# Kernel tuning notes

Measured on AMD Instinct MI355X. Metric: run time of the kernel, lower is better.

## Reference

```python
import jax, jax.numpy as jnp
import numpy as np
import math

N_PATHS = 2048
N_STEPS = 512
N_FWD = 40
N_FACTORS = 3
H = 0.1
ALPHA = H - 0.5            # fBM kernel exponent
BETA_SABR = 0.5
SHIFT = 0.02
DT = 1.0 / N_STEPS
GAMMA_CONST = math.gamma(H + 0.5)
BETA_DECAY = 0.05


def setup_inputs() -> dict:
    key = jax.random.key(0)
    tenors = np.linspace(0.0, 10.0, N_FWD + 1)
    T = tenors[:-1]
    tau = np.diff(tenors).astype(np.float32)
    F0 = np.full(N_FWD, 0.02, dtype=np.float32)
    # alphas = base normal vols / |F0+shift|^beta  (as in __init__)
    base_vols = np.full(N_FWD, 0.006)
    eta_F0 = np.abs(F0 + SHIFT) ** BETA_SABR
    alphas = (base_vols / eta_F0).astype(np.float32)
    rhos = np.full(N_FWD, -0.3, dtype=np.float32)
    nus = np.full(N_FWD, 0.5, dtype=np.float32)
    # PCA loadings from exponential spatial correlation (as in __init__)
    corr = np.exp(-BETA_DECAY * np.abs(T[:, None] - T[None, :]))
    evals, evecs = np.linalg.eigh(corr)
    idx = np.argsort(evals)[::-1][:N_FACTORS]
    L = evecs[:, idx] * np.sqrt(np.clip(evals[idx], 0.0, None))[None, :]
    L = L / np.sqrt((L ** 2).sum(axis=1, keepdims=True))
    Lam = np.triu(L @ L.T, 1).astype(np.float32)
    # Brownian increments, pre-scaled by sqrt(dt) (replaces Sobol+icdf draw)
    dz = jax.random.normal(key, (N_PATHS, N_STEPS, N_FACTORS + 1), dtype=jnp.float32) * float(np.sqrt(DT))
    return {
        "dz_all": dz,
        "F0": jnp.asarray(F0),
        "alphas": jnp.asarray(alphas),
        "rhos": jnp.asarray(rhos),
        "nus": jnp.asarray(nus),
        "tau": jnp.asarray(tau),
        "loadings": jnp.asarray(L.astype(np.float32)),
        "Lambda_upper": jnp.asarray(Lam),
    }


def reference(dz_all, F0, alphas, rhos, nus, tau, loadings, Lambda_upper):
    n_paths, n_steps, _ = dz_all.shape
    dtype = dz_all.dtype
    # --- hybrid-scheme Volterra / fBM kernel [n_steps, n_steps] ---
    idx = jnp.arange(n_steps)
    k = jnp.maximum(idx[:, None] - idx[None, :] + 1, 0).astype(dtype)
    # with b_eval='optimal', riemann == exact weights, so the where(k<=kappa) is identity
    exact_w = (k ** (ALPHA + 1.0) - jnp.maximum(k - 1.0, 0.0) ** (ALPHA + 1.0)) / (ALPHA + 1.0)
    kernel = jnp.where(idx[:, None] >= idx[None, :], exact_w * (DT ** ALPHA) / GAMMA_CONST, 0.0)
    # variance compensator [N, n_steps]
    var_comp = 0.5 * (nus ** 2)[:, None] * jnp.sum(kernel ** 2, axis=1)[None, :] * DT
    # --- correlated Brownian drivers and fBM via kernel convolution ---
    wr = jnp.einsum('psf,nf->psn', dz_all[..., :N_FACTORS], loadings)          # [P,S,N]
    fbm4 = jnp.einsum('ts,psd->ptd', kernel, dz_all)                            # [P,S,4]
    fbm_curve = jnp.einsum('ptf,nf->ptn', fbm4[..., :N_FACTORS], loadings)      # [P,S,N]
    fbm = rhos * fbm_curve + jnp.sqrt(1.0 - rhos ** 2) * fbm4[..., -1:]
    unit_vols = jnp.exp(nus * fbm - var_comp.T[None])                            # [P,S,N]
    v2_dt = unit_vols ** 2 * DT
    # --- frozen-drift forward dynamics ---
    eta_f0 = jnp.abs(F0 + SHIFT) ** BETA_SABR
    vol_scale = alphas * eta_f0
    omega_0 = tau * vol_scale / (1.0 + tau * F0)
    mu_0 = -vol_scale * (Lambda_upper @ omega_0)
    dF = mu_0 * v2_dt + wr * (unit_vols * vol_scale)
    F_path = F0 + jnp.cumsum(dF, axis=1)                                         # [P,S,N]
    return jnp.concatenate([jnp.broadcast_to(F0, (n_paths, 1, F0.shape[0])), F_path], axis=1)
```

## Files before the change

kernel.cpp:

```cpp
#include <hip/hip_runtime.h>
#include <math.h>

#define NS 512
#define NF 40
#define ROWS_OUT 513
#define DTC (1.0f / 512.0f)
#define PLANE 512


__global__ __launch_bounds__(64) void const_kernel(
    const float* __restrict__ F0, const float* __restrict__ alphas,
    const float* __restrict__ rhos, const float* __restrict__ nus,
    const float* __restrict__ tau, const float* __restrict__ L,
    const float* __restrict__ Lam, float* __restrict__ ws)
{
    __shared__ double wd[NS];
    __shared__ float omega0[NF];
    __shared__ float vs_s[NF];
    int n = threadIdx.x;

    {
        const double g06 = 1.4891922488128171;
        const double dta = pow(512.0, 0.4);
        #pragma unroll
        for (int k = 0; k < 8; ++k) {
            int m = n * 8 + k;
            double wv = (pow((double)m + 1.0, 0.6) - pow((double)m, 0.6)) * (1.0 / 0.6) * dta / g06;
            wd[m] = wv;
            ws[m] = (float)wv;
        }
    }
    if (n < NF) {
        float f0 = F0[n];
        float vs = alphas[n] * sqrtf(fabsf(f0 + 0.02f));
        vs_s[n] = vs;
        omega0[n] = tau[n] * vs / (1.0f + tau[n] * f0);
    }
    __syncthreads();
    if (n == 0) {
        double acc = 0.0;
        for (int m = 0; m < NS; ++m) { acc += wd[m] * wd[m]; ws[NS + m] = (float)acc; }
    }
    if (n < NF) {
        float s = 0.0f;
        for (int j = 0; j < NF; ++j) s += Lam[n * NF + j] * omega0[j];
        float vs = vs_s[n];
        float mu0 = -vs * s;
        float rho = rhos[n], nu = nus[n];
        float* c = ws + 1024 + n * 8;
        c[0] = vs * L[n * 3 + 0];
        c[1] = vs * L[n * 3 + 1];
        c[2] = vs * L[n * 3 + 2];
        c[3] = nu * rho / fmaxf(vs, 1e-30f);
        c[4] = nu * sqrtf(fmaxf(1.0f - rho * rho, 0.0f));
        c[5] = 0.5f * nu * nu * DTC;
        c[6] = mu0 * DTC;
        c[7] = F0[n];
    }
}

template<int CTRL, int RM>
__device__ __forceinline__ float dpp_add(float v) {
    int t = __builtin_amdgcn_update_dpp(0, __float_as_int(v), CTRL, RM, 0xf, true);
    return v + __int_as_float(t);
}
__device__ __forceinline__ float wave_iscan(float v) {
    v = dpp_add<0x111, 0xf>(v);
    v = dpp_add<0x112, 0xf>(v);
    v = dpp_add<0x114, 0xf>(v);
    v = dpp_add<0x118, 0xf>(v);
    v = dpp_add<0x142, 0xa>(v);
    v = dpp_add<0x143, 0xc>(v);
    return v;
}

__device__ __forceinline__ void fma4(float4& acc, float c, const float4& v) {
    acc.x = fmaf(c, v.x, acc.x);
    acc.y = fmaf(c, v.y, acc.y);
    acc.z = fmaf(c, v.z, acc.z);
    acc.w = fmaf(c, v.w, acc.w);
}

__global__ __launch_bounds__(256, 8) void path_kernel(
    const float* __restrict__ dz, const float* __restrict__ ws,
    float* __restrict__ out)
{
    __shared__ float planes[4 * PLANE];
    __shared__ float ustage[64 * 41];

    int tid = threadIdx.x;
    int lane = tid & 63;
    int wv = __builtin_amdgcn_readfirstlane(tid >> 6);
    int p = blockIdx.x;
    const float4* dzg = (const float4*)dz + (size_t)p * NS;

    float* wp = ustage;
    for (int i = tid; i < 768; i += 256) wp[i] = (i < 256) ? 0.0f : ws[i - 256];
    __syncthreads();

    {
        int role = (wv + p) & 3;
        int half = role >> 1;
        int seg  = role & 1;
        int i = half * 64 + lane;
        int span = half ? 64 : 32;
        int g0 = seg * span, g1 = g0 + span;
        const float4* wp4 = (const float4*)wp;
        float4 a0 = make_float4(0.f, 0.f, 0.f, 0.f);
        float4 a1 = a0, a2 = a0, a3 = a0;
        #pragma unroll 2
        for (int g = g0; g < g1; ++g) {
            float4 d0 = dzg[4 * g + 0];
            float4 d1 = dzg[4 * g + 1];
            float4 d2 = dzg[4 * g + 2];
            float4 d3 = dzg[4 * g + 3];
            float4 lo = wp4[63 + i - g];
            float4 hi = wp4[64 + i - g];
            fma4(a0, hi.x, d0); fma4(a1, hi.y, d0); fma4(a2, hi.z, d0); fma4(a3, hi.w, d0);
            fma4(a0, lo.w, d1); fma4(a1, hi.x, d1); fma4(a2, hi.y, d1); fma4(a3, hi.z, d1);
            fma4(a0, lo.z, d2); fma4(a1, lo.w, d2); fma4(a2, hi.x, d2); fma4(a3, hi.y, d2);
            fma4(a0, lo.y, d3); fma4(a1, lo.z, d3); fma4(a2, lo.w, d3); fma4(a3, hi.x, d3);
        }
        if (seg == 1) {
            ((float4*)(planes + 0 * PLANE))[i] = make_float4(a0.x, a1.x, a2.x, a3.x);
            ((float4*)(planes + 1 * PLANE))[i] = make_float4(a0.y, a1.y, a2.y, a3.y);
            ((float4*)(planes + 2 * PLANE))[i] = make_float4(a0.z, a1.z, a2.z, a3.z);
            ((float4*)(planes + 3 * PLANE))[i] = make_float4(a0.w, a1.w, a2.w, a3.w);
        }
        __syncthreads();
        if (seg == 0) {
            float4* q0 = &((float4*)(planes + 0 * PLANE))[i];
            float4* q1 = &((float4*)(planes + 1 * PLANE))[i];
            float4* q2 = &((float4*)(planes + 2 * PLANE))[i];
            float4* q3 = &((float4*)(planes + 3 * PLANE))[i];
            float4 c0 = *q0, c1 = *q1, c2 = *q2, c3 = *q3;
            c0.x += a0.x; c0.y += a1.x; c0.z += a2.x; c0.w += a3.x;
            c1.x += a0.y; c1.y += a1.y; c1.z += a2.y; c1.w += a3.y;
            c2.x += a0.z; c2.y += a1.z; c2.z += a2.z; c2.w += a3.z;
            c3.x += a0.w; c3.y += a1.w; c3.z += a2.w; c3.w += a3.w;
            *q0 = c0; *q1 = c1; *q2 = c2; *q3 = c3;
        }
        __syncthreads();
    }

    float carry[10];
    #pragma unroll
    for (int j = 0; j < 10; ++j) carry[j] = 0.0f;

    float* outP = out + (size_t)p * (ROWS_OUT * NF);
    if (tid < NF) outP[tid] = ws[1024 + tid * 8 + 7];

    float* chunk = ustage;
    const float* cwg = ws + NS;
    for (int cix = 0; cix < 8; ++cix) {
        int t = cix * 64 + lane;
        float cw = cwg[t];
        float fx = planes[t], fy = planes[PLANE + t];
        float fz = planes[2 * PLANE + t], fw = planes[3 * PLANE + t];
        float4 d = dzg[t];
        #pragma unroll
        for (int j = 0; j < 10; ++j) {
            int n = wv * 10 + j;
            const float* c = ws + 1024 + n * 8;
            float cC0 = c[0], cC1 = c[1], cC2 = c[2], q = c[3];
            float cA3 = c[4], ca = c[5], cm0 = c[6], f0 = c[7];
            float dotf = fx * cC0 + fy * cC1 + fz * cC2;
            float arg = fmaf(q, dotf, fmaf(cA3, fw, -ca * cw));
            float uv = __expf(arg);
            float dotc = d.x * cC0 + d.y * cC1 + d.z * cC2;
            float dF = uv * fmaf(cm0, uv, dotc);
            float v = wave_iscan(dF) + carry[j];
            carry[j] = __int_as_float(__builtin_amdgcn_readlane(__float_as_int(v), 63));
            chunk[lane * 41 + n] = v + f0;
        }
        __syncthreads();
        float* o = outP + NF + cix * (64 * NF);
        #pragma unroll
        for (int k = 0; k < 10; ++k) {
            int f = tid + k * 256;
            __builtin_nontemporal_store(chunk[f + f / 40], o + f);
        }
        __syncthreads();
    }
}

extern "C" void kernel_launch(void* const* d_in, const int* in_sizes, int n_in,
                              void* d_out, int out_size, void* d_ws, size_t ws_size,
                              hipStream_t stream) {
    const float* dz   = (const float*)d_in[0];
    const float* F0   = (const float*)d_in[1];
    const float* alph = (const float*)d_in[2];
    const float* rhos = (const float*)d_in[3];
    const float* nus  = (const float*)d_in[4];
    const float* tau  = (const float*)d_in[5];
    const float* L    = (const float*)d_in[6];
    const float* Lam  = (const float*)d_in[7];
    float* ws = (float*)d_ws;
    float* out = (float*)d_out;

    int n_paths = in_sizes[0] / (NS * 4);

    const_kernel<<<1, 64, 0, stream>>>(F0, alph, rhos, nus, tau, L, Lam, ws);
    path_kernel<<<n_paths, 256, 0, stream>>>(dz, ws, out);
}
```

Measured before the change: 256.2 us.

## Compute fBM kernel convolution with bf16 MFMA over a materialized Toeplitz matrix

```diff
diff --git a/kernel.cpp b/kernel.cpp
--- a/kernel.cpp
+++ b/kernel.cpp
@@ -7,6 +7,15 @@
 #define DTC (1.0f / 512.0f)
 #define PLANE 512
 
+typedef short bf16x8 __attribute__((ext_vector_type(8)));
+typedef float f32x4 __attribute__((ext_vector_type(4)));
+
+#define W_BYTES_NEEDED (1344u * 4u + 512u * 512u * 2u)
+
+__device__ __forceinline__ unsigned short f2bf(float x) {
+    unsigned int u = __float_as_uint(x);
+    return (unsigned short)((u + 0x7FFFu + ((u >> 16) & 1u)) >> 16);
+}
 
 __global__ __launch_bounds__(64) void const_kernel(
     const float* __restrict__ F0, const float* __restrict__ alphas,
@@ -18,7 +27,6 @@
     __shared__ float omega0[NF];
     __shared__ float vs_s[NF];
     int n = threadIdx.x;
-
     {
         const double g06 = 1.4891922488128171;
         const double dta = pow(512.0, 0.4);
@@ -59,6 +67,19 @@
     }
 }
 
+__global__ __launch_bounds__(128) void toeplitz_kernel(float* __restrict__ ws)
+{
+    int t = blockIdx.x;
+    int s0 = threadIdx.x * 4;
+    ushort4 v;
+    v.x = (s0 + 0 <= t) ? f2bf(ws[t - s0 - 0]) : (unsigned short)0;
+    v.y = (s0 + 1 <= t) ? f2bf(ws[t - s0 - 1]) : (unsigned short)0;
+    v.z = (s0 + 2 <= t) ? f2bf(ws[t - s0 - 2]) : (unsigned short)0;
+    v.w = (s0 + 3 <= t) ? f2bf(ws[t - s0 - 3]) : (unsigned short)0;
+    ushort4* W = (ushort4*)((unsigned short*)(ws + 1344) + (size_t)t * 512);
+    W[threadIdx.x] = v;
+}
+
 template<int CTRL, int RM>
 __device__ __forceinline__ float dpp_add(float v) {
     int t = __builtin_amdgcn_update_dpp(0, __float_as_int(v), CTRL, RM, 0xf, true);
@@ -79,6 +100,105 @@
     acc.y = fmaf(c, v.y, acc.y);
     acc.z = fmaf(c, v.z, acc.z);
     acc.w = fmaf(c, v.w, acc.w);
+}
+
+__global__ __launch_bounds__(256, 8) void path_kernel_mfma(
+    const float* __restrict__ dz, const float* __restrict__ ws,
+    float* __restrict__ out)
+{
+    __shared__ float planes[NS * 4];
+    __shared__ float ustage[64 * 41];
+
+    int tid = threadIdx.x;
+    int lane = tid & 63;
+    int wv = __builtin_amdgcn_readfirstlane(tid >> 6);
+    int p = blockIdx.x;
+    const float4* dzg = (const float4*)dz + (size_t)p * NS;
+
+    unsigned short* dzb = (unsigned short*)ustage;
+    {
+        int k2 = tid * 2;
+        float4 da = dzg[k2], db = dzg[k2 + 1];
+        unsigned int* d32 = (unsigned int*)dzb;
+        d32[0 * 256 + tid] = (unsigned int)f2bf(da.x) | ((unsigned int)f2bf(db.x) << 16);
+        d32[1 * 256 + tid] = (unsigned int)f2bf(da.y) | ((unsigned int)f2bf(db.y) << 16);
+        d32[2 * 256 + tid] = (unsigned int)f2bf(da.z) | ((unsigned int)f2bf(db.z) << 16);
+        d32[3 * 256 + tid] = (unsigned int)f2bf(da.w) | ((unsigned int)f2bf(db.w) << 16);
+    }
+    __syncthreads();
+
+    {
+        const unsigned short* W = (const unsigned short*)(ws + 1344);
+        int arow = lane & 15, ksub = lane >> 4;
+        f32x4 acc[8];
+        #pragma unroll
+        for (int j = 0; j < 8; ++j) acc[j] = (f32x4){0.f, 0.f, 0.f, 0.f};
+        const unsigned short* bbase = dzb + (lane & 3) * 512 + ksub * 8;
+        #pragma unroll 1
+        for (int k = 0; k < 16; ++k) {
+            bf16x8 bf = *(const bf16x8*)(bbase + k * 32);
+            #pragma unroll
+            for (int j = 0; j < 8; ++j) {
+                int m = wv + 4 * j;
+                if (k <= ((16 * m + 15) >> 5)) {
+                    bf16x8 af = *(const bf16x8*)(W + (size_t)(16 * m + arow) * NS + k * 32 + ksub * 8);
+                    acc[j] = __builtin_amdgcn_mfma_f32_16x16x32_bf16(af, bf, acc[j], 0, 0, 0);
+                }
+            }
+        }
+        if (arow < 4) {
+            #pragma unroll
+            for (int j = 0; j < 8; ++j) {
+                int m = wv + 4 * j;
+                #pragma unroll
+                for (int r = 0; r < 4; ++r)
+                    planes[(16 * m + ksub * 4 + r) * 4 + arow] = acc[j][r];
+            }
+        }
+    }
+
+    float carry[10];
+    #pragma unroll
+    for (int j = 0; j < 10; ++j) carry[j] = 0.0f;
+
+    float* outP = out + (size_t)p * (ROWS_OUT * NF);
+    if (tid < NF) outP[tid] = ws[1024 + tid * 8 + 7];
+
+    __syncthreads();
+
+    float* chunk = ustage;
+    const float* cwg = ws + NS;
+    const float4* planes4 = (const float4*)planes;
+    for (int cix = 0; cix < 8; ++cix) {
+        int t = cix * 64 + lane;
+        float cw = cwg[t];
+        float4 f4 = planes4[t];
+        float fx = f4.x, fy = f4.y, fz = f4.z, fw = f4.w;
+        float4 d = dzg[t];
+        #pragma unroll
+        for (int j = 0; j < 10; ++j) {
+            int n = wv * 10 + j;
+            const float* c = ws + 1024 + n * 8;
+            float cC0 = c[0], cC1 = c[1], cC2 = c[2], q = c[3];
+            float cA3 = c[4], ca = c[5], cm0 = c[6], f0 = c[7];
+            float dotf = fx * cC0 + fy * cC1 + fz * cC2;
+            float arg = fmaf(q, dotf, fmaf(cA3, fw, -ca * cw));
+            float uv = __expf(arg);
+            float dotc = d.x * cC0 + d.y * cC1 + d.z * cC2;
+            float dF = uv * fmaf(cm0, uv, dotc);
+            float v = wave_iscan(dF) + carry[j];
+            carry[j] = __int_as_float(__builtin_amdgcn_readlane(__float_as_int(v), 63));
+            chunk[lane * 41 + n] = v + f0;
+        }
+        __syncthreads();
+        float* o = outP + NF + cix * (64 * NF);
+        #pragma unroll
+        for (int k = 0; k < 10; ++k) {
+            int f = tid + k * 256;
+            __builtin_nontemporal_store(chunk[f + f / 40], o + f);
+        }
+        __syncthreads();
+    }
 }
 
 __global__ __launch_bounds__(256, 8) void path_kernel(
@@ -201,5 +321,10 @@
     int n_paths = in_sizes[0] / (NS * 4);
 
     const_kernel<<<1, 64, 0, stream>>>(F0, alph, rhos, nus, tau, L, Lam, ws);
-    path_kernel<<<n_paths, 256, 0, stream>>>(dz, ws, out);
-}
+    if (ws_size >= (size_t)W_BYTES_NEEDED) {
+        toeplitz_kernel<<<512, 128, 0, stream>>>(ws);
+        path_kernel_mfma<<<n_paths, 256, 0, stream>>>(dz, ws, out);
+    } else {
+        path_kernel<<<n_paths, 256, 0, stream>>>(dz, ws, out);
+    }
+}
```

Measured after the change: 280.5 us. 9.5% more time.
